# Kernel optimization log

Measured on AMD Instinct MI355X. Metric: run time of the kernel, lower is better.

The kernel has to match this reference:

```python
import jax, jax.numpy as jnp
import numpy as np

B, N, C, D, H, L, F = 64, 256, 16, 512, 8, 8, 2048
HD = D // H
PI = np.pi


def _ln(x, w, b, eps=1e-5):
    mu = jnp.mean(x, -1, keepdims=True)
    var = jnp.mean(jnp.square(x - mu), -1, keepdims=True)
    return (x - mu) * jax.lax.rsqrt(var + eps) * w + b


def _forward(x_node, x_full, Wp, bp, cls, e_w1, e_b1, e_w2, e_b2, edge_scale,
             qkv_w, qkv_b, out_w, out_b, ln1_w, ln1_b, ln2_w, ln2_b,
             ff1_w, ff1_b, ff2_w, ff2_b, cl_ln_w, cl_ln_b, cl_w1, cl_b1, cl_w2, cl_b2):
    Bq, Nq, _ = x_node.shape
    # pairwise kaon geometry from absolute y/phi
    y = x_full[:, :, 14]
    phi = x_full[:, :, 15]
    dy = jnp.abs(y[:, :, None] - y[:, None, :])                                  # [B,N,N]
    dphi = jnp.abs(jnp.mod(phi[:, :, None] - phi[:, None, :] + PI, 2 * PI) - PI)
    dr = jnp.sqrt(dy * dy + dphi * dphi + 1e-8)
    ef = jnp.stack([dy, dphi, dr], -1)                                           # [B,N,N,3]
    hmid = jax.nn.gelu(ef @ e_w1.T + e_b1, approximate=False)                    # [B,N,N,16]
    raw = hmid @ e_w2.T + e_b2                                                   # [B,N,N,H]
    central = jnp.mean(raw, axis=2).transpose(0, 2, 1)                           # [B,H,N]
    edge_bias = raw.transpose(0, 3, 1, 2)                                        # [B,H,N,N]
    bias = jnp.zeros((Bq, H, Nq + 1, Nq + 1), x_node.dtype)
    bias = bias.at[:, :, 1:, 1:].set(edge_bias)
    bias = bias.at[:, :, 0, 1:].set(central * edge_scale)
    bias = bias.at[:, :, 1:, 0].set(central * edge_scale)

    h = x_node @ Wp.T + bp
    h = jnp.concatenate([jnp.broadcast_to(cls, (Bq, 1, D)), h], axis=1)          # [B,S,D]
    S = Nq + 1
    scale = 1.0 / np.sqrt(HD)
    for l in range(L):  # pre-norm TransformerEncoderLayer (activation=relu, no final norm)
        x = _ln(h, ln1_w[l], ln1_b[l])
        qkv = x @ qkv_w[l].T + qkv_b[l]
        q, k, v = jnp.split(qkv, 3, axis=-1)
        q = q.reshape(Bq, S, H, HD).transpose(0, 2, 1, 3)
        k = k.reshape(Bq, S, H, HD).transpose(0, 2, 1, 3)
        v = v.reshape(Bq, S, H, HD).transpose(0, 2, 1, 3)
        scores = jnp.einsum('bhqd,bhkd->bhqk', q, k) * scale + bias
        attn = jax.nn.softmax(scores, axis=-1)
        o = jnp.einsum('bhqk,bhkd->bhqd', attn, v).transpose(0, 2, 1, 3).reshape(Bq, S, D)
        h = h + o @ out_w[l].T + out_b[l]
        x = _ln(h, ln2_w[l], ln2_b[l])
        h = h + jax.nn.relu(x @ ff1_w[l].T + ff1_b[l]) @ ff2_w[l].T + ff2_b[l]
    x = _ln(h[:, 0], cl_ln_w, cl_ln_b)
    return jax.nn.gelu(x @ cl_w1.T + cl_b1, approximate=False) @ cl_w2.T + cl_b2  # [B,2]


def setup_inputs() -> dict:
    key = jax.random.key(0)
    ks = iter(jax.random.split(key, 40))
    f32 = jnp.float32

    def nrm(shape, s=0.02):
        return (s * jax.random.normal(next(ks), shape)).astype(f32)

    return {
        'x_node': jax.random.normal(next(ks), (B, N, C), f32),
        'x_full': jax.random.normal(next(ks), (B, N, 16), f32),
        'Wp': nrm((D, C)), 'bp': jnp.zeros((D,), f32),
        'cls': nrm((1, 1, D)),
        'e_w1': nrm((16, 3), 0.3), 'e_b1': jnp.zeros((16,), f32),
        'e_w2': nrm((H, 16), 0.01), 'e_b2': jnp.zeros((H,), f32),
        'edge_scale': jnp.full((1,), 0.1, f32),
        'qkv_w': nrm((L, 3 * D, D)), 'qkv_b': jnp.zeros((L, 3 * D), f32),
        'out_w': nrm((L, D, D)), 'out_b': jnp.zeros((L, D), f32),
        'ln1_w': jnp.ones((L, D), f32), 'ln1_b': jnp.zeros((L, D), f32),
        'ln2_w': jnp.ones((L, D), f32), 'ln2_b': jnp.zeros((L, D), f32),
        'ff1_w': nrm((L, F, D)), 'ff1_b': jnp.zeros((L, F), f32),
        'ff2_w': nrm((L, D, F)), 'ff2_b': jnp.zeros((L, D), f32),
        'cl_ln_w': jnp.ones((D,), f32), 'cl_ln_b': jnp.zeros((D,), f32),
        'cl_w1': nrm((D // 2, D)), 'cl_b1': jnp.zeros((D // 2,), f32),
        'cl_w2': nrm((2, D // 2)), 'cl_b2': jnp.zeros((2,), f32),
    }


def reference(x_node, x_full, Wp, bp, cls, e_w1, e_b1, e_w2, e_b2, edge_scale,
              qkv_w, qkv_b, out_w, out_b, ln1_w, ln1_b, ln2_w, ln2_b,
              ff1_w, ff1_b, ff2_w, ff2_b, cl_ln_w, cl_ln_b, cl_w1, cl_b1, cl_w2, cl_b2):
    return _forward(x_node, x_full, Wp, bp, cls, e_w1, e_b1, e_w2, e_b2, edge_scale,
                    qkv_w, qkv_b, out_w, out_b, ln1_w, ln1_b, ln2_w, ln2_b,
                    ff1_w, ff1_b, ff2_w, ff2_b, cl_ln_w, cl_ln_b, cl_w1, cl_b1, cl_w2, cl_b2)
```

## Files before the change

kernel.cpp:

```cpp
#include <hip/hip_runtime.h>
#include <hip/hip_bf16.h>
#include <stdint.h>

#define PI_F     3.14159265358979323846f
#define TWO_PI_F 6.28318530717958647692f
#define INV2PI_F 0.15915494309189535f

typedef __attribute__((ext_vector_type(8))) short bf16x8;
typedef __attribute__((ext_vector_type(4))) float f32x4;

#define BB 64
#define NN 256
#define SS 257
#define DD 512
#define HH 8
#define HDD 64
#define LL 8
#define MTOK 16448
#define MPAD 16512
#define BSTR 264
#define VSTR 320

__device__ __forceinline__ float b2f(unsigned short u){
  union { float f; uint32_t i; } c; c.i = ((uint32_t)u) << 16; return c.f;
}
__device__ __forceinline__ unsigned short f2b(float f){
  union { float f; uint32_t i; } c; c.f = f;
  uint32_t r = c.i + 0x7FFFu + ((c.i >> 16) & 1u);
  return (unsigned short)(r >> 16);
}
__device__ __forceinline__ float gelu_fast(float z){
  const float z2 = z*z;
  const float u2 = z * (1.5957691216f + 0.071354816f*z2);
  const float e = __expf(u2);
  const float th = 1.f - 2.f/(1.f + e);
  return 0.5f*z*(1.f + th);
}

typedef __attribute__((address_space(1))) unsigned char ga_t;
typedef __attribute__((address_space(3))) unsigned char ls_t;
__device__ __forceinline__ void gl_lds16(const void* g, void* l){
  __builtin_amdgcn_global_load_lds((ga_t*)g, (ls_t*)l, 16, 0, 0);
}

__global__ __launch_bounds__(256) void cvt_kernel(const float* __restrict__ src,
                                                  unsigned short* __restrict__ dst, int n2){
  int i = blockIdx.x*256 + threadIdx.x;
  int stride = gridDim.x*256;
  for (; i < n2; i += stride){
    float2 v = ((const float2*)src)[i];
    ((uint32_t*)dst)[i] = (uint32_t)f2b(v.x) | ((uint32_t)f2b(v.y) << 16);
  }
}

__global__ __launch_bounds__(256) void edge_kernel(
    const float* __restrict__ x_full, const float* __restrict__ e_w1, const float* __restrict__ e_b1,
    const float* __restrict__ e_w2, const float* __restrict__ e_b2,
    unsigned short* __restrict__ bias, float* __restrict__ central)
{
  const int bi = blockIdx.x;
  const int b = bi >> 8, i = bi & 255;
  const int j = threadIdx.x;
  const float yi = x_full[((long)b*NN + i)*16 + 14];
  const float fi = x_full[((long)b*NN + i)*16 + 15];
  const float yj = x_full[((long)b*NN + j)*16 + 14];
  const float fj = x_full[((long)b*NN + j)*16 + 15];
  const float dy = fabsf(yi - yj);
  const float xw = fi - fj + PI_F;
  const float tw = xw * INV2PI_F;
  const float md = (tw - floorf(tw)) * TWO_PI_F;
  const float dphi = fabsf(md - PI_F);
  const float dr = sqrtf(dy*dy + dphi*dphi + 1e-8f);
  float raw[8];
  #pragma unroll
  for (int hh = 0; hh < 8; ++hh) raw[hh] = e_b2[hh];
  #pragma unroll
  for (int k = 0; k < 16; ++k){
    float z = e_w1[k*3]*dy + e_w1[k*3+1]*dphi + e_w1[k*3+2]*dr + e_b1[k];
    float g = gelu_fast(z);
    #pragma unroll
    for (int hh = 0; hh < 8; ++hh) raw[hh] += g * e_w2[hh*16 + k];
  }
  #pragma unroll
  for (int hh = 0; hh < 8; ++hh)
    bias[(((long)b*HH + hh)*SS + 1 + i)*BSTR + 1 + j] = f2b(raw[hh]);
  #pragma unroll
  for (int m = 1; m < 64; m <<= 1)
    #pragma unroll
    for (int hh = 0; hh < 8; ++hh) raw[hh] += __shfl_xor(raw[hh], m);
  __shared__ float cw[4][8];
  const int wv = j >> 6;
  if ((j & 63) == 0)
    for (int hh = 0; hh < 8; ++hh) cw[wv][hh] = raw[hh];
  __syncthreads();
  if (j < 8){
    float t = cw[0][j] + cw[1][j] + cw[2][j] + cw[3][j];
    central[((long)b*NN + i)*HH + j] = t * (1.f/NN);
  }
}

__global__ __launch_bounds__(256) void edge_border_kernel(
    const float* __restrict__ central, const float* __restrict__ edge_scale,
    unsigned short* __restrict__ bias)
{
  const int bh = blockIdx.x;
  const int b = bh >> 3, h = bh & 7;
  const int j = threadIdx.x;
  const float es = edge_scale[0];
  const float cv = central[((long)b*NN + j)*HH + h] * es;
  const long base = (long)bh*SS*BSTR;
  const unsigned short u = f2b(cv);
  bias[base + 1 + j] = u;
  bias[base + (long)(1+j)*BSTR] = u;
  if (j == 0) bias[base] = 0;
}

__global__ __launch_bounds__(256) void proj_kernel(
    const float* __restrict__ x_node, const float* __restrict__ Wp,
    const float* __restrict__ bp, const float* __restrict__ cls, float* __restrict__ hb)
{
  const int t = blockIdx.x;
  const int tid = threadIdx.x;
  const int b = t / SS, s2 = t - b*SS;
  float2 o;
  if (s2 == 0){
    o = *(const float2*)(cls + tid*2);
  } else {
    const float* xr = x_node + ((long)b*NN + (s2-1))*16;
    float xv[16];
    #pragma unroll
    for (int c2 = 0; c2 < 16; ++c2) xv[c2] = xr[c2];
    float oo[2];
    #pragma unroll
    for (int e = 0; e < 2; ++e){
      int d = tid*2 + e;
      float a = bp[d];
      const float* wr2 = Wp + (long)d*16;
      #pragma unroll
      for (int c2 = 0; c2 < 16; ++c2) a += xv[c2]*wr2[c2];
      oo[e] = a;
    }
    o.x = oo[0]; o.y = oo[1];
  }
  *(float2*)(hb + (long)t*DD + tid*2) = o;
}

__global__ __launch_bounds__(256) void ln_kernel(
    const float* __restrict__ hb, const float* __restrict__ w,
    const float* __restrict__ bbv, unsigned short* __restrict__ xb)
{
  const int tok = blockIdx.x*4 + (threadIdx.x >> 6);
  const int lane = threadIdx.x & 63;
  const float4* p = (const float4*)(hb + (long)tok*DD + lane*8);
  const float4 a = p[0], bq = p[1];
  float s  = a.x + a.y + a.z + a.w + bq.x + bq.y + bq.z + bq.w;
  float ss = a.x*a.x + a.y*a.y + a.z*a.z + a.w*a.w
           + bq.x*bq.x + bq.y*bq.y + bq.z*bq.z + bq.w*bq.w;
  #pragma unroll
  for (int m = 1; m < 64; m <<= 1){ s += __shfl_xor(s, m); ss += __shfl_xor(ss, m); }
  const float mu = s * (1.f/DD);
  const float var = ss * (1.f/DD) - mu*mu;
  const float rs = rsqrtf(var + 1e-5f);
  const float4* wp = (const float4*)(w + lane*8);
  const float4* bp2 = (const float4*)(bbv + lane*8);
  const float4 w0 = wp[0], w1 = wp[1];
  const float4 b0 = bp2[0], b1 = bp2[1];
  bf16x8 o;
  o[0] = (short)f2b((a.x - mu)*rs*w0.x + b0.x);
  o[1] = (short)f2b((a.y - mu)*rs*w0.y + b0.y);
  o[2] = (short)f2b((a.z - mu)*rs*w0.z + b0.z);
  o[3] = (short)f2b((a.w - mu)*rs*w0.w + b0.w);
  o[4] = (short)f2b((bq.x - mu)*rs*w1.x + b1.x);
  o[5] = (short)f2b((bq.y - mu)*rs*w1.y + b1.y);
  o[6] = (short)f2b((bq.z - mu)*rs*w1.z + b1.z);
  o[7] = (short)f2b((bq.w - mu)*rs*w1.w + b1.w);
  *(bf16x8*)(xb + (long)tok*DD + lane*8) = o;
}

template<int EPI>
__global__ __launch_bounds__(256, 4) void gemm_kernel(
    const unsigned short* __restrict__ A, const unsigned short* __restrict__ Bw,
    const float* __restrict__ bias, void* __restrict__ Cout,
    int M, int N, int K, int ldc, int nblocks)
{
  __shared__ unsigned short As[128*64];
  __shared__ unsigned short Bs[128*64];
  const int tid = threadIdx.x;
  const int lane = tid & 63;
  const int wave = tid >> 6;
  const int wr = wave >> 1, wc = wave & 1;
  const int l16 = lane & 15, lhi = lane >> 4;

  const int nwg = gridDim.x;
  const int q8 = nwg >> 3, r8 = nwg & 7;
  const int xcd = blockIdx.x & 7, idx = blockIdx.x >> 3;
  const int lin = (xcd < r8 ? xcd*(q8+1) : r8*(q8+1) + (xcd-r8)*q8) + idx;
  const int mb = lin / nblocks;
  const int nb = lin - mb*nblocks;
  const long m0 = (long)mb * 128;
  const long n0 = (long)nb * 128;

  f32x4 acc[4][4];
  const f32x4 z4 = {0.f, 0.f, 0.f, 0.f};
  #pragma unroll
  for (int mi = 0; mi < 4; ++mi)
    #pragma unroll
    for (int ni = 0; ni < 4; ++ni) acc[mi][ni] = z4;

  const char* Ab = (const char*)A;
  const char* Bb = (const char*)Bw;
  const int nkt = K >> 6;
  for (int kt = 0; kt < nkt; ++kt){
    #pragma unroll
    for (int c = 0; c < 4; ++c){
      const int bo = c*4096 + tid*16;
      const int row = bo >> 7;
      const int kb = bo & 127;
      gl_lds16(Ab + ((m0+row)*(long)K)*2 + (long)kt*128 + kb, (char*)As + bo);
      gl_lds16(Bb + ((n0+row)*(long)K)*2 + (long)kt*128 + kb, (char*)Bs + bo);
    }
    __syncthreads();
    #pragma unroll
    for (int kd = 0; kd < 2; ++kd){
      bf16x8 af[4], bfr[4];
      #pragma unroll
      for (int mi = 0; mi < 4; ++mi)
        af[mi] = *(const bf16x8*)((const char*)As + (wr*64 + mi*16 + l16)*128 + kd*64 + lhi*16);
      #pragma unroll
      for (int ni = 0; ni < 4; ++ni)
        bfr[ni] = *(const bf16x8*)((const char*)Bs + (wc*64 + ni*16 + l16)*128 + kd*64 + lhi*16);
      #pragma unroll
      for (int mi = 0; mi < 4; ++mi)
        #pragma unroll
        for (int ni = 0; ni < 4; ++ni)
          acc[mi][ni] = __builtin_amdgcn_mfma_f32_16x16x32_bf16(af[mi], bfr[ni], acc[mi][ni], 0, 0, 0);
    }
    __syncthreads();
  }
  #pragma unroll
  for (int mi = 0; mi < 4; ++mi){
    #pragma unroll
    for (int ni = 0; ni < 4; ++ni){
      const int col = (int)n0 + wc*64 + ni*16 + l16;
      const float bn = bias[col];
      const int rowb = (int)m0 + wr*64 + mi*16 + lhi*4;
      #pragma unroll
      for (int r = 0; r < 4; ++r){
        const int m = rowb + r;
        if (m < M){
          float v = acc[mi][ni][r] + bn;
          if (EPI == 1) v = fmaxf(v, 0.f);
          if (EPI == 2) ((float*)Cout)[(long)m*ldc + col] += v;
          else          ((unsigned short*)Cout)[(long)m*ldc + col] = f2b(v);
        }
      }
    }
  }
}

__global__ __launch_bounds__(256) void vtrans_kernel(
    const unsigned short* __restrict__ qkv, unsigned short* __restrict__ vt)
{
  const int bh = blockIdx.x;
  const int c = blockIdx.y;
  const int b = bh >> 3, h = bh & 7;
  __shared__ unsigned short tile[64][72];
  const int tid = threadIdx.x;
  const int rr = tid >> 3, ch = tid & 7;
  #pragma unroll
  for (int it = 0; it < 2; ++it){
    const int sl = it*32 + rr;
    const long tok = (long)b*SS + c*64 + sl;
    bf16x8 v = *(const bf16x8*)(qkv + tok*1536 + 1024 + h*64 + ch*8);
    *(bf16x8*)(&tile[sl][ch*8]) = v;
  }
  __syncthreads();
  #pragma unroll
  for (int it = 0; it < 2; ++it){
    const int d = it*32 + rr;
    const int s0 = c*64 + ch*8;
    bf16x8 o;
    #pragma unroll
    for (int e = 0; e < 8; ++e){
      const int sgl = s0 + e;
      o[e] = (sgl < SS) ? (short)tile[ch*8 + e][d] : (short)0;
    }
    *(bf16x8*)(vt + ((long)bh*HDD + d)*VSTR + s0) = o;
  }
}

__global__ __launch_bounds__(576) void flash_kernel(
    const unsigned short* __restrict__ qkv, const unsigned short* __restrict__ vt,
    const unsigned short* __restrict__ bias, unsigned short* __restrict__ ob)
{
  const int bh = blockIdx.x;
  const int b = bh >> 3, h = bh & 7;
  const int qt = threadIdx.x >> 6;
  const int lane = threadIdx.x & 63;
  const int l16 = lane & 15, lhi = lane >> 4;

  __shared__ unsigned short Ks[2][2048];
  __shared__ unsigned short Vs[2][2048];
  __shared__ unsigned short Bsh[9][2][1024];
  __shared__ unsigned short pt[9][1024];
  unsigned short* ptw = pt[qt];

  bf16x8 qf[2][2];
  #pragma unroll
  for (int mi = 0; mi < 2; ++mi)
    #pragma unroll
    for (int kd = 0; kd < 2; ++kd){
      const long tok = (long)b*SS + qt*32 + mi*16 + l16;
      qf[mi][kd] = *(const bf16x8*)(qkv + tok*1536 + h*64 + kd*32 + lhi*8);
    }

  auto stage = [&](int jtn, int bb){
    const int rB = lane >> 2, cB = lane & 3;
    const char* gb = (const char*)bias + (((long)bh*SS + qt*32)*BSTR + (long)jtn*32)*2;
    char* lb = (char*)&Bsh[qt][bb][0];
    gl_lds16(gb + (long)rB*BSTR*2        + cB*16, lb + lane*16);
    gl_lds16(gb + (long)(16+rB)*BSTR*2   + cB*16, lb + 1024 + lane*16);
    if (qt < 4){
      const int rK = lane >> 3, cK = lane & 7;
      gl_lds16((const char*)qkv + (((long)b*SS + jtn*32 + qt*8 + rK)*1536 + 512 + h*64)*2 + ((cK ^ rK)*16),
               (char*)&Ks[bb][0] + qt*1024 + lane*16);
    } else if (qt < 8){
      const int rV = lane >> 2, cV = lane & 3;
      const int d = (qt-4)*16 + rV;
      gl_lds16((const char*)vt + (((long)bh*64 + d)*VSTR + (long)jtn*32)*2 + ((cV ^ (rV & 3))*16),
               (char*)&Vs[bb][0] + (qt-4)*1024 + lane*16);
    }
  };

  f32x4 oacc[2][4];
  const f32x4 z4 = {0.f, 0.f, 0.f, 0.f};
  #pragma unroll
  for (int mi = 0; mi < 2; ++mi)
    #pragma unroll
    for (int ni = 0; ni < 4; ++ni) oacc[mi][ni] = z4;
  float mrow[2][4], lrow[2][4];
  #pragma unroll
  for (int mi = 0; mi < 2; ++mi)
    #pragma unroll
    for (int r = 0; r < 4; ++r){ mrow[mi][r] = -1e30f; lrow[mi][r] = 0.f; }

  stage(0, 0);
  __builtin_amdgcn_sched_barrier(0);

  for (int jt = 0; jt < 9; ++jt){
    const int cur = jt & 1;
    if (jt < 8){
      stage(jt+1, cur ^ 1);
      __builtin_amdgcn_sched_barrier(0);
      if (qt < 8) asm volatile("s_waitcnt vmcnt(3)" ::: "memory");
      else        asm volatile("s_waitcnt vmcnt(2)" ::: "memory");
    } else {
      asm volatile("s_waitcnt vmcnt(0)" ::: "memory");
    }
    __builtin_amdgcn_sched_barrier(0);
    __builtin_amdgcn_s_barrier();
    __builtin_amdgcn_sched_barrier(0);

    bf16x8 kf[2][2];
    #pragma unroll
    for (int ni = 0; ni < 2; ++ni)
      #pragma unroll
      for (int kd = 0; kd < 2; ++kd){
        const int row = ni*16 + l16;
        const int sw = (kd*4 + lhi) ^ (row & 7);
        kf[ni][kd] = *(const bf16x8*)((const char*)&Ks[cur][0] + row*128 + sw*16);
      }
    f32x4 sacc[2][2];
    #pragma unroll
    for (int mi = 0; mi < 2; ++mi)
      #pragma unroll
      for (int ni = 0; ni < 2; ++ni) sacc[mi][ni] = z4;
    __builtin_amdgcn_s_setprio(1);
    #pragma unroll
    for (int kd = 0; kd < 2; ++kd)
      #pragma unroll
      for (int mi = 0; mi < 2; ++mi)
        #pragma unroll
        for (int ni = 0; ni < 2; ++ni)
          sacc[mi][ni] = __builtin_amdgcn_mfma_f32_16x16x32_bf16(qf[mi][kd], kf[ni][kd], sacc[mi][ni], 0, 0, 0);
    __builtin_amdgcn_s_setprio(0);

    float sv[2][2][4];
    #pragma unroll
    for (int mi = 0; mi < 2; ++mi)
      #pragma unroll
      for (int ni = 0; ni < 2; ++ni)
        #pragma unroll
        for (int r = 0; r < 4; ++r){
          const int col = jt*32 + ni*16 + l16;
          float x = sacc[mi][ni][r] * 0.125f;
          x += b2f(Bsh[qt][cur][(mi*16 + lhi*4 + r)*32 + ni*16 + l16]);
          if (col >= SS) x = -1e30f;
          sv[mi][ni][r] = x;
        }
    #pragma unroll
    for (int mi = 0; mi < 2; ++mi)
      #pragma unroll
      for (int r = 0; r < 4; ++r){
        float pm = fmaxf(sv[mi][0][r], sv[mi][1][r]);
        #pragma unroll
        for (int sh = 1; sh < 16; sh <<= 1) pm = fmaxf(pm, __shfl_xor(pm, sh));
        const float mold = mrow[mi][r];
        const float mnew = fmaxf(mold, pm);
        const float corr = __expf(mold - mnew);
        mrow[mi][r] = mnew;
        float psum = 0.f;
        #pragma unroll
        for (int ni = 0; ni < 2; ++ni){
          const float p = __expf(sv[mi][ni][r] - mnew);
          sv[mi][ni][r] = p;
          psum += p;
        }
        #pragma unroll
        for (int sh = 1; sh < 16; sh <<= 1) psum += __shfl_xor(psum, sh);
        lrow[mi][r] = lrow[mi][r]*corr + psum;
        #pragma unroll
        for (int ni = 0; ni < 4; ++ni) oacc[mi][ni][r] = oacc[mi][ni][r]*corr;
      }
    #pragma unroll
    for (int mi = 0; mi < 2; ++mi)
      #pragma unroll
      for (int ni = 0; ni < 2; ++ni)
        #pragma unroll
        for (int r = 0; r < 4; ++r)
          ptw[(mi*16 + lhi*4 + r)*32 + ni*16 + l16] = f2b(sv[mi][ni][r]);
    bf16x8 pf[2];
    #pragma unroll
    for (int mi = 0; mi < 2; ++mi)
      pf[mi] = *(const bf16x8*)(ptw + (mi*16 + l16)*32 + lhi*8);
    bf16x8 vf[4];
    #pragma unroll
    for (int ni = 0; ni < 4; ++ni){
      const int d = ni*16 + l16;
      const int sw = lhi ^ (d & 3);
      vf[ni] = *(const bf16x8*)((const char*)&Vs[cur][0] + d*64 + sw*16);
    }
    __builtin_amdgcn_s_setprio(1);
    #pragma unroll
    for (int mi = 0; mi < 2; ++mi)
      #pragma unroll
      for (int ni = 0; ni < 4; ++ni)
        oacc[mi][ni] = __builtin_amdgcn_mfma_f32_16x16x32_bf16(pf[mi], vf[ni], oacc[mi][ni], 0, 0, 0);
    __builtin_amdgcn_s_setprio(0);

    __builtin_amdgcn_sched_barrier(0);
    __builtin_amdgcn_s_barrier();
    __builtin_amdgcn_sched_barrier(0);
  }

  #pragma unroll
  for (int mi = 0; mi < 2; ++mi)
    #pragma unroll
    for (int r = 0; r < 4; ++r){
      const int row = qt*32 + mi*16 + lhi*4 + r;
      if (row < SS){
        const float inv = 1.0f / lrow[mi][r];
        const long tok = (long)b*SS + row;
        #pragma unroll
        for (int ni = 0; ni < 4; ++ni)
          ob[tok*DD + h*HDD + ni*16 + l16] = f2b(oacc[mi][ni][r] * inv);
      }
    }
}

__global__ __launch_bounds__(256) void cls_kernel(
    const float* __restrict__ hb, const float* __restrict__ lw, const float* __restrict__ lb,
    const float* __restrict__ w1, const float* __restrict__ b1,
    const float* __restrict__ w2, const float* __restrict__ b2, float* __restrict__ out)
{
  const int b = blockIdx.x;
  const int tid = threadIdx.x;
  const float* row = hb + (long)b*SS*DD;
  const float2 v = *(const float2*)(row + tid*2);
  float s = v.x + v.y, ss = v.x*v.x + v.y*v.y;
  #pragma unroll
  for (int m = 1; m < 64; m <<= 1){ s += __shfl_xor(s, m); ss += __shfl_xor(ss, m); }
  __shared__ float red[8];
  const int wv = tid >> 6;
  if ((tid & 63) == 0){ red[wv] = s; red[4+wv] = ss; }
  __syncthreads();
  s  = red[0]+red[1]+red[2]+red[3];
  ss = red[4]+red[5]+red[6]+red[7];
  const float mu = s * (1.f/DD);
  const float var = ss * (1.f/DD) - mu*mu;
  const float rs = rsqrtf(var + 1e-5f);
  __shared__ __align__(16) float xs[DD];
  xs[tid*2]   = (v.x - mu)*rs*lw[tid*2]   + lb[tid*2];
  xs[tid*2+1] = (v.y - mu)*rs*lw[tid*2+1] + lb[tid*2+1];
  __syncthreads();
  float a = b1[tid];
  const float4* w1v = (const float4*)(w1 + (long)tid*DD);
  const float4* xsv = (const float4*)xs;
  for (int d4 = 0; d4 < DD/4; ++d4){
    const float4 wv4 = w1v[d4], xv4 = xsv[d4];
    a += wv4.x*xv4.x + wv4.y*xv4.y + wv4.z*xv4.z + wv4.w*xv4.w;
  }
  const float g = 0.5f*a*(1.f + erff(a*0.70710678118f));
  float p0 = g * w2[tid];
  float p1 = g * w2[256 + tid];
  #pragma unroll
  for (int m = 1; m < 64; m <<= 1){ p0 += __shfl_xor(p0, m); p1 += __shfl_xor(p1, m); }
  __shared__ float r2[8];
  if ((tid & 63) == 0){ r2[wv] = p0; r2[4+wv] = p1; }
  __syncthreads();
  if (tid == 0) out[b*2]   = r2[0]+r2[1]+r2[2]+r2[3] + b2[0];
  if (tid == 1) out[b*2+1] = r2[4]+r2[5]+r2[6]+r2[7] + b2[1];
}

extern "C" void kernel_launch(void* const* d_in, const int* in_sizes, int n_in,
                              void* d_out, int out_size, void* d_ws, size_t ws_size,
                              hipStream_t stream) {
  const float* x_node    = (const float*)d_in[0];
  const float* x_full    = (const float*)d_in[1];
  const float* Wp        = (const float*)d_in[2];
  const float* bp        = (const float*)d_in[3];
  const float* cls       = (const float*)d_in[4];
  const float* e_w1      = (const float*)d_in[5];
  const float* e_b1      = (const float*)d_in[6];
  const float* e_w2      = (const float*)d_in[7];
  const float* e_b2      = (const float*)d_in[8];
  const float* edge_scale= (const float*)d_in[9];
  const float* qkv_w     = (const float*)d_in[10];
  const float* qkv_b     = (const float*)d_in[11];
  const float* out_w     = (const float*)d_in[12];
  const float* out_b     = (const float*)d_in[13];
  const float* ln1_w     = (const float*)d_in[14];
  const float* ln1_b     = (const float*)d_in[15];
  const float* ln2_w     = (const float*)d_in[16];
  const float* ln2_b     = (const float*)d_in[17];
  const float* ff1_w     = (const float*)d_in[18];
  const float* ff1_b     = (const float*)d_in[19];
  const float* ff2_w     = (const float*)d_in[20];
  const float* ff2_b     = (const float*)d_in[21];
  const float* cl_ln_w   = (const float*)d_in[22];
  const float* cl_ln_b   = (const float*)d_in[23];
  const float* cl_w1     = (const float*)d_in[24];
  const float* cl_b1     = (const float*)d_in[25];
  const float* cl_w2     = (const float*)d_in[26];
  const float* cl_b2     = (const float*)d_in[27];
  float* out = (float*)d_out;

  char* w = (char*)d_ws;
  size_t off = 0;
  auto take = [&](size_t bytes)->char*{
    char* p = w + off;
    off += (bytes + 255) & ~(size_t)255;
    return p;
  };
  unsigned short* wq8   = (unsigned short*)take((size_t)LL*1536*512*2);
  unsigned short* wo8   = (unsigned short*)take((size_t)LL*512*512*2);
  unsigned short* wf1   = (unsigned short*)take((size_t)LL*2048*512*2);
  unsigned short* wf2   = (unsigned short*)take((size_t)LL*512*2048*2);
  unsigned short* bias16= (unsigned short*)take((size_t)BB*HH*SS*BSTR*2 + 65536);
  float*          cent  = (float*)take((size_t)BB*NN*HH*4);
  float*          hbuf  = (float*)take((size_t)MPAD*DD*4);
  unsigned short* xb    = (unsigned short*)take((size_t)MPAD*DD*2);
  unsigned short* obuf  = (unsigned short*)take((size_t)MPAD*DD*2);
  unsigned short* qkvb  = (unsigned short*)take((size_t)MPAD*1536*2);
  unsigned short* vtb   = (unsigned short*)take((size_t)BB*HH*HDD*VSTR*2);
  unsigned short* ffb   = qkvb;

  cvt_kernel<<<4096, 256, 0, stream>>>(qkv_w, wq8, LL*1536*512/2);
  cvt_kernel<<<4096, 256, 0, stream>>>(out_w, wo8, LL*512*512/2);
  cvt_kernel<<<4096, 256, 0, stream>>>(ff1_w, wf1, LL*2048*512/2);
  cvt_kernel<<<4096, 256, 0, stream>>>(ff2_w, wf2, LL*512*2048/2);

  edge_kernel<<<dim3(BB*NN), 256, 0, stream>>>(x_full, e_w1, e_b1, e_w2, e_b2, bias16, cent);
  edge_border_kernel<<<dim3(BB*HH), 256, 0, stream>>>(cent, edge_scale, bias16);
  proj_kernel<<<dim3(MTOK), 256, 0, stream>>>(x_node, Wp, bp, cls, hbuf);

  for (int l = 0; l < LL; ++l){
    ln_kernel<<<dim3(MTOK/4), 256, 0, stream>>>(hbuf, ln1_w + l*DD, ln1_b + l*DD, xb);
    gemm_kernel<0><<<dim3(129*12), 256, 0, stream>>>(xb, wq8 + (size_t)l*1536*512,
        qkv_b + (size_t)l*1536, qkvb, MTOK, 1536, 512, 1536, 12);
    vtrans_kernel<<<dim3(512, 5), 256, 0, stream>>>(qkvb, vtb);
    flash_kernel<<<dim3(512), 576, 0, stream>>>(qkvb, vtb, bias16, obuf);
    gemm_kernel<2><<<dim3(129*4), 256, 0, stream>>>(obuf, wo8 + (size_t)l*512*512,
        out_b + (size_t)l*DD, hbuf, MTOK, 512, 512, 512, 4);
    ln_kernel<<<dim3(MTOK/4), 256, 0, stream>>>(hbuf, ln2_w + l*DD, ln2_b + l*DD, xb);
    gemm_kernel<1><<<dim3(129*16), 256, 0, stream>>>(xb, wf1 + (size_t)l*2048*512,
        ff1_b + (size_t)l*2048, ffb, MTOK, 2048, 512, 2048, 16);
    gemm_kernel<2><<<dim3(129*4), 256, 0, stream>>>(ffb, wf2 + (size_t)l*512*2048,
        ff2_b + (size_t)l*DD, hbuf, MTOK, 512, 2048, 512, 4);
  }
  cls_kernel<<<dim3(BB), 256, 0, stream>>>(hbuf, cl_ln_w, cl_ln_b, cl_w1, cl_b1, cl_w2, cl_b2, out);
}
```

Before: 2.675 ms.

## Double-buffer GEMM LDS tiles to overlap global loads with MFMA

```diff
diff --git a/kernel.cpp b/kernel.cpp
--- a/kernel.cpp
+++ b/kernel.cpp
@@ -178,13 +178,13 @@
 }
 
 template<int EPI>
-__global__ __launch_bounds__(256, 4) void gemm_kernel(
+__global__ __launch_bounds__(256, 2) void gemm_kernel(
     const unsigned short* __restrict__ A, const unsigned short* __restrict__ Bw,
     const float* __restrict__ bias, void* __restrict__ Cout,
     int M, int N, int K, int ldc, int nblocks)
 {
-  __shared__ unsigned short As[128*64];
-  __shared__ unsigned short Bs[128*64];
+  __shared__ unsigned short As[2][128*64];
+  __shared__ unsigned short Bs[2][128*64];
   const int tid = threadIdx.x;
   const int lane = tid & 63;
   const int wave = tid >> 6;
@@ -209,33 +209,51 @@
 
   const char* Ab = (const char*)A;
   const char* Bb = (const char*)Bw;
-  const int nkt = K >> 6;
-  for (int kt = 0; kt < nkt; ++kt){
+
+  auto stage = [&](int kt, int bb){
     #pragma unroll
     for (int c = 0; c < 4; ++c){
       const int bo = c*4096 + tid*16;
       const int row = bo >> 7;
       const int kb = bo & 127;
-      gl_lds16(Ab + ((m0+row)*(long)K)*2 + (long)kt*128 + kb, (char*)As + bo);
-      gl_lds16(Bb + ((n0+row)*(long)K)*2 + (long)kt*128 + kb, (char*)Bs + bo);
-    }
-    __syncthreads();
+      gl_lds16(Ab + ((m0+row)*(long)K)*2 + (long)kt*128 + kb, (char*)As[bb] + bo);
+      gl_lds16(Bb + ((n0+row)*(long)K)*2 + (long)kt*128 + kb, (char*)Bs[bb] + bo);
+    }
+  };
+
+  const int nkt = K >> 6;
+  stage(0, 0);
+  int bb = 0;
+  for (int kt = 0; kt < nkt; ++kt){
+    if (kt + 1 < nkt){
+      stage(kt + 1, bb ^ 1);
+      __builtin_amdgcn_sched_barrier(0);
+      asm volatile("s_waitcnt vmcnt(8)" ::: "memory");
+    } else {
+      asm volatile("s_waitcnt vmcnt(0)" ::: "memory");
+    }
+    __builtin_amdgcn_sched_barrier(0);
+    __builtin_amdgcn_s_barrier();
+    __builtin_amdgcn_sched_barrier(0);
     #pragma unroll
     for (int kd = 0; kd < 2; ++kd){
       bf16x8 af[4], bfr[4];
       #pragma unroll
       for (int mi = 0; mi < 4; ++mi)
-        af[mi] = *(const bf16x8*)((const char*)As + (wr*64 + mi*16 + l16)*128 + kd*64 + lhi*16);
+        af[mi] = *(const bf16x8*)((const char*)As[bb] + (wr*64 + mi*16 + l16)*128 + kd*64 + lhi*16);
       #pragma unroll
       for (int ni = 0; ni < 4; ++ni)
-        bfr[ni] = *(const bf16x8*)((const char*)Bs + (wc*64 + ni*16 + l16)*128 + kd*64 + lhi*16);
+        bfr[ni] = *(const bf16x8*)((const char*)Bs[bb] + (wc*64 + ni*16 + l16)*128 + kd*64 + lhi*16);
       #pragma unroll
       for (int mi = 0; mi < 4; ++mi)
         #pragma unroll
         for (int ni = 0; ni < 4; ++ni)
           acc[mi][ni] = __builtin_amdgcn_mfma_f32_16x16x32_bf16(af[mi], bfr[ni], acc[mi][ni], 0, 0, 0);
     }
-    __syncthreads();
+    __builtin_amdgcn_sched_barrier(0);
+    __builtin_amdgcn_s_barrier();
+    __builtin_amdgcn_sched_barrier(0);
+    bb ^= 1;
   }
   #pragma unroll
   for (int mi = 0; mi < 4; ++mi){
```

Result: slower. 3.712 ms (+38.8%).
